# Kernel optimization log

Measured on AMD Instinct MI355X. Metric: run time of the kernel, lower is better.

Reference implementation:

```python
import jax, jax.numpy as jnp
import numpy as np

B, L, C, H = 2, 2048, 1024, 16  # batches, tokens per batch, channels, heads


def _ln(x, eps=1e-6):
    # LayerNorm32: no affine, eps=1e-6, computed in fp32
    x32 = x.astype(jnp.float32)
    m = x32.mean(-1, keepdims=True)
    v = ((x32 - m) ** 2).mean(-1, keepdims=True)
    return ((x32 - m) * jax.lax.rsqrt(v + eps)).astype(x.dtype)


def setup_inputs() -> dict:
    key = jax.random.key(0)
    ks = jax.random.split(key, 8)
    s = 0.02
    return {
        "feats": jax.random.normal(ks[0], (B * L, C), jnp.float32),
        "mod": jax.random.normal(ks[1], (B, C), jnp.float32),
        "w_mod": jax.random.normal(ks[2], (C, 6 * C), jnp.float32) * s,
        "b_mod": jnp.zeros((6 * C,), jnp.float32),
        "w_qkv": jax.random.normal(ks[3], (C, 3 * C), jnp.float32) * s,
        "b_qkv": jnp.zeros((3 * C,), jnp.float32),
        "w_proj": jax.random.normal(ks[4], (C, C), jnp.float32) * s,
        "b_proj": jnp.zeros((C,), jnp.float32),
        "w_fc1": jax.random.normal(ks[5], (C, 4 * C), jnp.float32) * s,
        "b_fc1": jnp.zeros((4 * C,), jnp.float32),
        "w_fc2": jax.random.normal(ks[6], (4 * C, C), jnp.float32) * s,
        "b_fc2": jnp.zeros((C,), jnp.float32),
        "seq_len": L,
    }


def reference(feats, mod, w_mod, b_mod, w_qkv, b_qkv, w_proj, b_proj,
              w_fc1, b_fc1, w_fc2, b_fc2, seq_len):
    Bn, Cn = mod.shape
    Ln = seq_len
    Hn = H
    D = Cn // Hn

    # adaLN modulation: SiLU -> Linear(C, 6C), chunk into 6 [B, C] pieces
    m = jax.nn.silu(mod) @ w_mod + b_mod
    sh_a, sc_a, g_a, sh_m, sc_m, g_m = jnp.split(m, 6, axis=1)

    x = feats.reshape(Bn, Ln, Cn)

    # --- MSA branch ---
    h = _ln(x)
    h = h * (1.0 + sc_a[:, None]) + sh_a[:, None]
    qkv = h @ w_qkv + b_qkv  # [B, L, 3C]
    q, k, v = [t.reshape(Bn, Ln, Hn, D) for t in jnp.split(qkv, 3, axis=-1)]
    scores = jnp.einsum('bqhd,bkhd->bhqk', q, k) / jnp.sqrt(jnp.float32(D))
    a = jax.nn.softmax(scores, axis=-1)
    o = jnp.einsum('bhqk,bkhd->bqhd', a, v).reshape(Bn, Ln, Cn)
    o = o @ w_proj + b_proj
    x = x + o * g_a[:, None]

    # --- FFN branch ---
    h = _ln(x)
    h = h * (1.0 + sc_m[:, None]) + sh_m[:, None]
    h = jax.nn.gelu(h @ w_fc1 + b_fc1, approximate=False) @ w_fc2 + b_fc2
    x = x + h * g_m[:, None]

    return x.reshape(Bn * Ln, Cn)
```

## Files before the change

kernel.cpp:

```cpp
#include <hip/hip_runtime.h>
#include <hip/hip_bf16.h>
#include <math.h>

#define B_ 2
#define L_ 2048
#define C_ 1024
#define H_ 16
#define D_ 64

typedef __attribute__((ext_vector_type(8))) short short8;
typedef __attribute__((ext_vector_type(4))) float float4v;

__device__ inline short f2bs(float f) {
    union { __hip_bfloat16 h; short s; } u; u.h = __float2bfloat16(f); return u.s;
}

#define GL2LDS(gp, lp)                                                         \
    __builtin_amdgcn_global_load_lds(                                          \
        (const __attribute__((address_space(1))) void*)(gp),                   \
        (__attribute__((address_space(3))) void*)(lp), 16, 0, 0)

__global__ __launch_bounds__(256) void k_mod2(const float* __restrict__ mod,
                                              const float* __restrict__ w_mod,
                                              const float* __restrict__ b_mod,
                                              float* __restrict__ m_out) {
    __shared__ float a_s[2][256];
    const int t = threadIdx.x;
    const int seg = blockIdx.y;
    for (int i = t; i < 512; i += 256) {
        float a = mod[(i >> 8) * C_ + seg * 256 + (i & 255)];
        a_s[i >> 8][i & 255] = a / (1.f + __expf(-a));
    }
    __syncthreads();
    int j = blockIdx.x * 256 + t;
    float acc0 = (seg == 0) ? b_mod[j] : 0.f;
    float acc1 = acc0;
    for (int k = 0; k < 256; ++k) {
        float w = w_mod[(size_t)(seg * 256 + k) * (6 * C_) + j];
        acc0 += a_s[0][k] * w;
        acc1 += a_s[1][k] * w;
    }
    atomicAdd(&m_out[j], acc0);
    atomicAdd(&m_out[6 * C_ + j], acc1);
}

__global__ __launch_bounds__(256) void k_wt_all(
        const float* __restrict__ w_qkv, const float* __restrict__ w_proj,
        const float* __restrict__ w_fc1, const float* __restrict__ w_fc2,
        short* __restrict__ wqkvT, short* __restrict__ wprojT,
        short* __restrict__ wfc1T, short* __restrict__ wfc2T) {
    __shared__ short T[64][72];
    int id = blockIdx.x;
    const float* W; short* WT; int K, N;
    if (id < 768)       {             W = w_qkv;  WT = wqkvT;  K = C_;     N = 3 * C_; }
    else if (id < 1024) { id -= 768;  W = w_proj; WT = wprojT; K = C_;     N = C_;     }
    else if (id < 2048) { id -= 1024; W = w_fc1;  WT = wfc1T;  K = C_;     N = 4 * C_; }
    else                { id -= 2048; W = w_fc2;  WT = wfc2T;  K = 4 * C_; N = C_;     }
    const int nb = N >> 6;
    const int n0 = (id % nb) * 64, k0 = (id / nb) * 64;
    const int t = threadIdx.x;
    {
        int kr = t >> 2, nc = (t & 3) * 16;
        const float* src = W + (size_t)(k0 + kr) * N + n0 + nc;
#pragma unroll
        for (int j = 0; j < 16; ++j) T[kr][nc + j] = f2bs(src[j]);
    }
    __syncthreads();
    {
        int nr = t >> 2, kc = (t & 3) * 16;
        short8 o0, o1;
#pragma unroll
        for (int j = 0; j < 8; ++j) { o0[j] = T[kc + j][nr]; o1[j] = T[kc + 8 + j][nr]; }
        short* dst = WT + (size_t)(n0 + nr) * K + k0 + kc;
        *(short8*)dst = o0;
        *(short8*)(dst + 8) = o1;
    }
}

__global__ __launch_bounds__(256) void k_vt(const __hip_bfloat16* __restrict__ qkv,
                                            short* __restrict__ vt) {
    __shared__ short T[64][72];
    const int t = threadIdx.x;
    const int kt = blockIdx.x * 64;
    const int bh = blockIdx.y;
    const int h = bh & (H_ - 1), b = bh >> 4;
    const __hip_bfloat16* src = qkv + ((size_t)(b * L_ + kt)) * (3 * C_) + 2 * C_ + h * D_;
    {
        int kr = t >> 2, dg = (t & 3) * 16;
        const short8* s = (const short8*)(src + (size_t)kr * (3 * C_) + dg);
        *(short8*)&T[kr][dg] = s[0];
        *(short8*)&T[kr][dg + 8] = s[1];
    }
    __syncthreads();
    {
        int dr = t >> 2, kg = (t & 3) * 16;
        short8 o0, o1;
#pragma unroll
        for (int j = 0; j < 8; ++j) { o0[j] = T[kg + j][dr]; o1[j] = T[kg + 8 + j][dr]; }
        short* dst = vt + ((size_t)bh * D_ + dr) * L_ + kt + kg;
        *(short8*)dst = o0;
        *(short8*)(dst + 8) = o1;
    }
}

__global__ __launch_bounds__(256) void k_ln_mod(const float* __restrict__ x,
                                                const float* __restrict__ mvec,
                                                int off_sh, int off_sc,
                                                __hip_bfloat16* __restrict__ h_out) {
    int row = blockIdx.x;
    int b = row / L_;
    int t = threadIdx.x;
    float v[4];
    float s = 0.f, ss = 0.f;
#pragma unroll
    for (int i = 0; i < 4; ++i) {
        int c = t + i * 256;
        float val = x[(size_t)row * C_ + c];
        v[i] = val; s += val; ss += val * val;
    }
#pragma unroll
    for (int o = 32; o; o >>= 1) { s += __shfl_xor(s, o); ss += __shfl_xor(ss, o); }
    __shared__ float red[2][4];
    int wid = t >> 6, lane = t & 63;
    if (lane == 0) { red[0][wid] = s; red[1][wid] = ss; }
    __syncthreads();
    s  = red[0][0] + red[0][1] + red[0][2] + red[0][3];
    ss = red[1][0] + red[1][1] + red[1][2] + red[1][3];
    float mean = s * (1.f / C_);
    float var  = ss * (1.f / C_) - mean * mean;
    float rstd = rsqrtf(var + 1e-6f);
#pragma unroll
    for (int i = 0; i < 4; ++i) {
        int c = t + i * 256;
        float sc = mvec[b * (6 * C_) + off_sc + c];
        float sh = mvec[b * (6 * C_) + off_sh + c];
        float hn = (v[i] - mean) * rstd;
        h_out[(size_t)row * C_ + c] = __float2bfloat16(hn * (1.f + sc) + sh);
    }
}

__device__ inline void gemm_epilogue(float v, int m, int n, int N, int act, int emode,
                                     const float* __restrict__ gate,
                                     const float* __restrict__ resid_f,
                                     __hip_bfloat16* __restrict__ out_bf,
                                     float* __restrict__ out_f) {
    if (act == 1) v = 0.5f * v * (1.f + erff(v * 0.70710678118654752440f));
    if (emode == 2) {
        float g = gate[(m >> 11) * (6 * C_) + n];
        v = resid_f[(size_t)m * N + n] + v * g;
    }
    if (out_f) out_f[(size_t)m * N + n] = v;
    else       out_bf[(size_t)m * N + n] = __float2bfloat16(v);
}

template<int WM, int WN, int MI, int NI>
__global__ __launch_bounds__(256) void k_gemm_async(
        const __hip_bfloat16* __restrict__ A, int lda,
        const short* __restrict__ WT, int ldw,
        const float* __restrict__ bias,
        int M, int N, int K, int act, int emode,
        const float* __restrict__ gate,
        const float* __restrict__ resid_f,
        __hip_bfloat16* __restrict__ out_bf,
        float* __restrict__ out_f) {
    constexpr int BM = WM * MI * 16;
    constexpr int BN = WN * NI * 16;
    __shared__ __align__(16) short A_lds[2][BM * 64];
    __shared__ __align__(16) short B_lds[2][BN * 64];
    const int t = threadIdx.x;
    const int lane = t & 63;
    const int w = t >> 6;
    const int wm = w / WN, wn = w % WN;
    const int quad = lane >> 4, l16 = lane & 15;
    const int m0 = blockIdx.y * BM;
    const int n0 = blockIdx.x * BN;

    auto stage = [&](int buf, int k0) {
#pragma unroll
        for (int rep = 0; rep < BM / 32; ++rep) {
            int p = rep * 256 + t;
            int row = p >> 3;
            int g = (p & 7) ^ (row & 7);
            const __hip_bfloat16* gp = A + (size_t)(m0 + row) * lda + k0 + g * 8;
            GL2LDS(gp, &A_lds[buf][(rep * 256 + (t & ~63)) * 8]);
        }
#pragma unroll
        for (int rep = 0; rep < BN / 32; ++rep) {
            int p = rep * 256 + t;
            int row = p >> 3;
            int g = (p & 7) ^ (row & 7);
            const short* gp = WT + (size_t)(n0 + row) * ldw + k0 + g * 8;
            GL2LDS(gp, &B_lds[buf][(rep * 256 + (t & ~63)) * 8]);
        }
    };

    float4v acc[MI][NI] = {};

    stage(0, 0);
    __syncthreads();

    const int nt = K >> 6;
    int cur = 0;
    for (int kt = 0; kt < nt; ++kt) {
        if (kt + 1 < nt) stage(cur ^ 1, (kt + 1) << 6);

        short8 af[MI][2], bfr[NI][2];
#pragma unroll
        for (int mi = 0; mi < MI; ++mi) {
            int r = wm * MI * 16 + mi * 16 + l16;
#pragma unroll
            for (int hh = 0; hh < 2; ++hh)
                af[mi][hh] = *(const short8*)(&A_lds[cur][(r * 8 + ((hh * 4 + quad) ^ (r & 7))) * 8]);
        }
#pragma unroll
        for (int ni = 0; ni < NI; ++ni) {
            int r = wn * NI * 16 + ni * 16 + l16;
#pragma unroll
            for (int hh = 0; hh < 2; ++hh)
                bfr[ni][hh] = *(const short8*)(&B_lds[cur][(r * 8 + ((hh * 4 + quad) ^ (r & 7))) * 8]);
        }
#pragma unroll
        for (int hh = 0; hh < 2; ++hh)
#pragma unroll
            for (int mi = 0; mi < MI; ++mi)
#pragma unroll
                for (int ni = 0; ni < NI; ++ni)
                    acc[mi][ni] = __builtin_amdgcn_mfma_f32_16x16x32_bf16(
                        af[mi][hh], bfr[ni][hh], acc[mi][ni], 0, 0, 0);

        __syncthreads();
        cur ^= 1;
    }

#pragma unroll
    for (int mi = 0; mi < MI; ++mi)
#pragma unroll
        for (int ni = 0; ni < NI; ++ni)
#pragma unroll
            for (int r = 0; r < 4; ++r) {
                int m = m0 + wm * MI * 16 + mi * 16 + quad * 4 + r;
                int n = n0 + wn * NI * 16 + ni * 16 + l16;
                float v = acc[mi][ni][r] + (bias ? bias[n] : 0.f);
                gemm_epilogue(v, m, n, N, act, emode, gate, resid_f, out_bf, out_f);
            }
}

__global__ __launch_bounds__(512) void k_attn(const __hip_bfloat16* __restrict__ qkv,
                                              const short* __restrict__ vt,
                                              __hip_bfloat16* __restrict__ o) {
    __shared__ __align__(16) short K_lds[2][64 * 72];
    __shared__ __align__(16) short V_lds[2][64 * 72];
    __shared__ __align__(16) short P_lds[8][16 * 72];
    const int t = threadIdx.x;
    const int lane = t & 63;
    const int w = t >> 6;
    const int quad = lane >> 4, l16 = lane & 15;

    const int raw = blockIdx.x;
    const int blk = (raw & 7) * 64 + (raw >> 3);
    const int bh = blk >> 4;
    const int q_blk = (blk & 15) * 128;
    const int h = bh & (H_ - 1);
    const int b = bh >> 4;

    const size_t stride = 3 * C_;
    const __hip_bfloat16* base = qkv + (size_t)b * L_ * stride + h * D_;

    short8 qf[2];
    {
        const __hip_bfloat16* qrow = base + (size_t)(q_blk + w * 16 + l16) * stride;
        qf[0] = *(const short8*)(qrow + quad * 8);
        qf[1] = *(const short8*)(qrow + 32 + quad * 8);
    }
    short8 ones;
#pragma unroll
    for (int j = 0; j < 8; ++j) ones[j] = (short)0x3F80;

    float4v o_acc[4];
    float4v l_acc = (float4v){0.f, 0.f, 0.f, 0.f};
#pragma unroll
    for (int dt = 0; dt < 4; ++dt) o_acc[dt] = (float4v){0.f, 0.f, 0.f, 0.f};

    const int s_row = t >> 3;
    const int s_col = (t & 7) * 8;
    const __hip_bfloat16* kg = base + C_;
    const short* vtb = vt + (size_t)bh * D_ * L_;

    short8 kreg = *(const short8*)(kg + (size_t)s_row * stride + s_col);
    short8 vreg = *(const short8*)(vtb + (size_t)s_row * L_ + s_col);
    *(short8*)&K_lds[0][s_row * 72 + s_col] = kreg;
    *(short8*)&V_lds[0][s_row * 72 + s_col] = vreg;
    __syncthreads();

    for (int kt = 0, cur = 0; kt < L_; kt += 64, cur ^= 1) {
        const int nxt = kt + 64;
        if (nxt < L_) {
            kreg = *(const short8*)(kg + (size_t)(nxt + s_row) * stride + s_col);
            vreg = *(const short8*)(vtb + (size_t)s_row * L_ + nxt + s_col);
        }

        float4v sacc[4];
        __builtin_amdgcn_s_setprio(1);
#pragma unroll
        for (int kb = 0; kb < 4; ++kb) {
            sacc[kb] = (float4v){0.f, 0.f, 0.f, 0.f};
            short8 kf0 = *(const short8*)(&K_lds[cur][(kb * 16 + l16) * 72 + quad * 8]);
            short8 kf1 = *(const short8*)(&K_lds[cur][(kb * 16 + l16) * 72 + 32 + quad * 8]);
            sacc[kb] = __builtin_amdgcn_mfma_f32_16x16x32_bf16(qf[0], kf0, sacc[kb], 0, 0, 0);
            sacc[kb] = __builtin_amdgcn_mfma_f32_16x16x32_bf16(qf[1], kf1, sacc[kb], 0, 0, 0);
        }
        __builtin_amdgcn_s_setprio(0);

#pragma unroll
        for (int r = 0; r < 4; ++r) {
            short* prow = &P_lds[w][(quad * 4 + r) * 72];
            prow[l16]      = f2bs(__expf(fmaf(sacc[0][r], 0.125f, -8.f)));
            prow[16 + l16] = f2bs(__expf(fmaf(sacc[1][r], 0.125f, -8.f)));
            prow[32 + l16] = f2bs(__expf(fmaf(sacc[2][r], 0.125f, -8.f)));
            prow[48 + l16] = f2bs(__expf(fmaf(sacc[3][r], 0.125f, -8.f)));
        }

        short8 pf0 = *(const short8*)(&P_lds[w][l16 * 72 + quad * 8]);
        short8 pf1 = *(const short8*)(&P_lds[w][l16 * 72 + 32 + quad * 8]);
        __builtin_amdgcn_s_setprio(1);
        l_acc = __builtin_amdgcn_mfma_f32_16x16x32_bf16(pf0, ones, l_acc, 0, 0, 0);
        l_acc = __builtin_amdgcn_mfma_f32_16x16x32_bf16(pf1, ones, l_acc, 0, 0, 0);
#pragma unroll
        for (int dt = 0; dt < 4; ++dt) {
            short8 vf0 = *(const short8*)(&V_lds[cur][(dt * 16 + l16) * 72 + quad * 8]);
            short8 vf1 = *(const short8*)(&V_lds[cur][(dt * 16 + l16) * 72 + 32 + quad * 8]);
            o_acc[dt] = __builtin_amdgcn_mfma_f32_16x16x32_bf16(pf0, vf0, o_acc[dt], 0, 0, 0);
            o_acc[dt] = __builtin_amdgcn_mfma_f32_16x16x32_bf16(pf1, vf1, o_acc[dt], 0, 0, 0);
        }
        __builtin_amdgcn_s_setprio(0);

        if (nxt < L_) {
            *(short8*)&K_lds[cur ^ 1][s_row * 72 + s_col] = kreg;
            *(short8*)&V_lds[cur ^ 1][s_row * 72 + s_col] = vreg;
        }
        __syncthreads();
    }

#pragma unroll
    for (int dt = 0; dt < 4; ++dt)
#pragma unroll
        for (int r = 0; r < 4; ++r) {
            int q = q_blk + w * 16 + quad * 4 + r;
            o[(size_t)(b * L_ + q) * C_ + h * D_ + dt * 16 + l16] =
                __float2bfloat16(o_acc[dt][r] / l_acc[r]);
        }
}

extern "C" void kernel_launch(void* const* d_in, const int* in_sizes, int n_in,
                              void* d_out, int out_size, void* d_ws, size_t ws_size,
                              hipStream_t stream) {
    const float* feats  = (const float*)d_in[0];
    const float* mod    = (const float*)d_in[1];
    const float* w_mod  = (const float*)d_in[2];
    const float* b_mod  = (const float*)d_in[3];
    const float* w_qkv  = (const float*)d_in[4];
    const float* b_qkv  = (const float*)d_in[5];
    const float* w_proj = (const float*)d_in[6];
    const float* b_proj = (const float*)d_in[7];
    const float* w_fc1  = (const float*)d_in[8];
    const float* b_fc1  = (const float*)d_in[9];
    const float* w_fc2  = (const float*)d_in[10];
    const float* b_fc2  = (const float*)d_in[11];

    const int M = B_ * L_;
    char* ws = (char*)d_ws;
    float* m_ws = (float*)ws;

    short* wqkvT  = (short*)(ws + 49152);
    short* wprojT = wqkvT + (size_t)3 * C_ * C_;
    short* wfc1T  = wprojT + (size_t)C_ * C_;
    short* wfc2T  = wfc1T + (size_t)4 * C_ * C_;
    char* slotB = (char*)(wfc2T + (size_t)4 * C_ * C_);
    __hip_bfloat16* qkv_ws = (__hip_bfloat16*)slotB;
    float* x1_ws           = (float*)slotB;
    __hip_bfloat16* slotA  = (__hip_bfloat16*)(slotB + (size_t)M * 3 * C_ * 2);
    __hip_bfloat16* hf_ws  = slotA + (size_t)M * C_;
    short* vt_ws           = (short*)hf_ws;

    k_wt_all<<<3072, 256, 0, stream>>>(w_qkv, w_proj, w_fc1, w_fc2,
                                       wqkvT, wprojT, wfc1T, wfc2T);
    hipMemsetAsync(m_ws, 0, 2 * 6 * C_ * sizeof(float), stream);
    k_mod2<<<dim3(24, 4), 256, 0, stream>>>(mod, w_mod, b_mod, m_ws);
    k_ln_mod<<<M, 256, 0, stream>>>(feats, m_ws, 0, 1024, slotA);
    k_gemm_async<2, 2, 4, 4><<<dim3(3 * C_ / 128, M / 128), 256, 0, stream>>>(
        slotA, C_, wqkvT, C_, b_qkv, M, 3 * C_, C_, 0, 0,
        nullptr, nullptr, qkv_ws, nullptr);
    k_vt<<<dim3(L_ / 64, B_ * H_), 256, 0, stream>>>(qkv_ws, vt_ws);
    k_attn<<<B_ * H_ * (L_ / 128), 512, 0, stream>>>(qkv_ws, vt_ws, slotA);
    k_gemm_async<4, 1, 2, 4><<<dim3(C_ / 64, M / 128), 256, 0, stream>>>(
        slotA, C_, wprojT, C_, b_proj, M, C_, C_, 0, 2,
        m_ws + 2 * C_, feats, nullptr, x1_ws);
    k_ln_mod<<<M, 256, 0, stream>>>(x1_ws, m_ws, 3 * C_, 4 * C_, slotA);
    k_gemm_async<2, 2, 4, 4><<<dim3(4 * C_ / 128, M / 128), 256, 0, stream>>>(
        slotA, C_, wfc1T, C_, b_fc1, M, 4 * C_, C_, 1, 0,
        nullptr, nullptr, hf_ws, nullptr);
    k_gemm_async<4, 1, 2, 4><<<dim3(C_ / 64, M / 128), 256, 0, stream>>>(
        hf_ws, 4 * C_, wfc2T, 4 * C_, b_fc2, M, C_, 4 * C_, 0, 2,
        m_ws + 5 * C_, x1_ws, nullptr, (float*)d_out);
}
```

Baseline: 489.0 us.

## Triple-buffer GEMM LDS with BK=32 and fine-grained vmcnt waits

Changes the async GEMM from a double-buffered K-tile of 64 to a triple-buffered K-tile of 32, prefetching two stages ahead. Instead of a full __syncthreads, which drains all outstanding loads, it uses explicit s_waitcnt vmcnt with the per-stage load count so that only the oldest stage must land before the barrier. The aim is to hide global-to-LDS latency better while keeping LDS usage about the same. In exchange there are twice as many barriers per K, each with less MFMA work between them, and correctness now depends on the hand-computed vmcnt count.

Measured after the change: 501.3 us. +2.5%, slower.

```diff
diff --git a/kernel.cpp b/kernel.cpp
--- a/kernel.cpp
+++ b/kernel.cpp
@@ -165,8 +165,9 @@
         float* __restrict__ out_f) {
     constexpr int BM = WM * MI * 16;
     constexpr int BN = WN * NI * 16;
-    __shared__ __align__(16) short A_lds[2][BM * 64];
-    __shared__ __align__(16) short B_lds[2][BN * 64];
+    constexpr int NLOADS = BM / 64 + BN / 64;
+    __shared__ __align__(16) short A_lds[3][BM * 32];
+    __shared__ __align__(16) short B_lds[3][BN * 32];
     const int t = threadIdx.x;
     const int lane = t & 63;
     const int w = t >> 6;
@@ -177,59 +178,69 @@
 
     auto stage = [&](int buf, int k0) {
 #pragma unroll
-        for (int rep = 0; rep < BM / 32; ++rep) {
+        for (int rep = 0; rep < BM / 64; ++rep) {
             int p = rep * 256 + t;
-            int row = p >> 3;
-            int g = (p & 7) ^ (row & 7);
+            int row = p >> 2;
+            int g = (p & 3) ^ (row & 3);
             const __hip_bfloat16* gp = A + (size_t)(m0 + row) * lda + k0 + g * 8;
             GL2LDS(gp, &A_lds[buf][(rep * 256 + (t & ~63)) * 8]);
         }
 #pragma unroll
-        for (int rep = 0; rep < BN / 32; ++rep) {
+        for (int rep = 0; rep < BN / 64; ++rep) {
             int p = rep * 256 + t;
-            int row = p >> 3;
-            int g = (p & 7) ^ (row & 7);
+            int row = p >> 2;
+            int g = (p & 3) ^ (row & 3);
             const short* gp = WT + (size_t)(n0 + row) * ldw + k0 + g * 8;
             GL2LDS(gp, &B_lds[buf][(rep * 256 + (t & ~63)) * 8]);
         }
     };
 
     float4v acc[MI][NI] = {};
+    const int nt = K >> 5;
 
     stage(0, 0);
-    __syncthreads();
-
-    const int nt = K >> 6;
-    int cur = 0;
+    if (nt > 1) {
+        stage(1, 32);
+        asm volatile("s_waitcnt vmcnt(%0)" :: "n"(NLOADS) : "memory");
+    } else {
+        asm volatile("s_waitcnt vmcnt(0)" ::: "memory");
+    }
+    __builtin_amdgcn_sched_barrier(0);
+    __builtin_amdgcn_s_barrier();
+    __builtin_amdgcn_sched_barrier(0);
+
+    int cur = 0, nx1 = 1, nx2 = 2;
     for (int kt = 0; kt < nt; ++kt) {
-        if (kt + 1 < nt) stage(cur ^ 1, (kt + 1) << 6);
-
-        short8 af[MI][2], bfr[NI][2];
+        if (kt + 2 < nt) stage(nx2, (kt + 2) << 5);
+
+        short8 af[MI], bfr[NI];
 #pragma unroll
         for (int mi = 0; mi < MI; ++mi) {
             int r = wm * MI * 16 + mi * 16 + l16;
-#pragma unroll
-            for (int hh = 0; hh < 2; ++hh)
-                af[mi][hh] = *(const short8*)(&A_lds[cur][(r * 8 + ((hh * 4 + quad) ^ (r & 7))) * 8]);
+            af[mi] = *(const short8*)(&A_lds[cur][(r * 4 + (quad ^ (r & 3))) * 8]);
         }
 #pragma unroll
         for (int ni = 0; ni < NI; ++ni) {
             int r = wn * NI * 16 + ni * 16 + l16;
-#pragma unroll
-            for (int hh = 0; hh < 2; ++hh)
-                bfr[ni][hh] = *(const short8*)(&B_lds[cur][(r * 8 + ((hh * 4 + quad) ^ (r & 7))) * 8]);
-        }
-#pragma unroll
-        for (int hh = 0; hh < 2; ++hh)
-#pragma unroll
-            for (int mi = 0; mi < MI; ++mi)
-#pragma unroll
-                for (int ni = 0; ni < NI; ++ni)
-                    acc[mi][ni] = __builtin_amdgcn_mfma_f32_16x16x32_bf16(
-                        af[mi][hh], bfr[ni][hh], acc[mi][ni], 0, 0, 0);
-
-        __syncthreads();
-        cur ^= 1;
+            bfr[ni] = *(const short8*)(&B_lds[cur][(r * 4 + (quad ^ (r & 3))) * 8]);
+        }
+#pragma unroll
+        for (int mi = 0; mi < MI; ++mi)
+#pragma unroll
+            for (int ni = 0; ni < NI; ++ni)
+                acc[mi][ni] = __builtin_amdgcn_mfma_f32_16x16x32_bf16(
+                    af[mi], bfr[ni], acc[mi][ni], 0, 0, 0);
+
+        if (kt + 1 < nt) {
+            if (kt + 2 < nt)
+                asm volatile("s_waitcnt vmcnt(%0)" :: "n"(NLOADS) : "memory");
+            else
+                asm volatile("s_waitcnt vmcnt(0)" ::: "memory");
+            __builtin_amdgcn_sched_barrier(0);
+            __builtin_amdgcn_s_barrier();
+            __builtin_amdgcn_sched_barrier(0);
+        }
+        int c = cur; cur = nx1; nx1 = nx2; nx2 = c;
     }
 
 #pragma unroll
```
